# Optimization experiments

Measured on AMD Instinct MI355X. Metric: run time of the kernel, lower is better.

## Reference

```python
import jax, jax.numpy as jnp
import numpy as np

SEQ, BATCH, HIDDEN, VOCAB = 2048, 2, 4096, 32000

def setup_inputs() -> dict:
    key = jax.random.key(0)
    k1, k2, k3 = jax.random.split(key, 3)
    hidden_states = jax.random.normal(k1, (SEQ, BATCH, HIDDEN), dtype=jnp.float32)
    weight = jax.random.normal(k2, (VOCAB, HIDDEN), dtype=jnp.float32) * (HIDDEN ** -0.5)
    labels = jax.random.randint(k3, (BATCH, SEQ), 0, VOCAB, dtype=jnp.int64)
    return {"hidden_states": hidden_states, "weight": weight, "labels": labels}

def reference(hidden_states, weight, labels):
    # LM head: [s,b,h] @ [v,h]^T -> [s,b,v]
    logits = jnp.einsum('sbh,vh->sbv', hidden_states, weight)
    labels_sb = labels.T  # [b,s] -> [s,b] to match logits layout
    # per-token cross entropy (vocab-parallel CE with world_size=1)
    logp = jax.nn.log_softmax(logits, axis=-1)
    nll = -jnp.take_along_axis(logp, labels_sb[..., None], axis=-1)[..., 0]  # [s,b]
    return nll.T  # [b,s], matching final loss.transpose(0,1)
```

## Files before the change

kernel.cpp:

```cpp
#include <hip/hip_runtime.h>
#include <hip/hip_bf16.h>
#include <stdint.h>

#define SEQ 2048
#define HID 4096
#define VOCAB 32000
#define MTOK 4096
#define NCHUNK 500

typedef __attribute__((ext_vector_type(8))) short short8v;
typedef __attribute__((ext_vector_type(4))) float float4v;

__device__ __forceinline__ short f2bf(float x) {
    unsigned u = __float_as_uint(x);
    u += 0x7fff + ((u >> 16) & 1);
    return (short)(u >> 16);
}

__global__ __launch_bounds__(256) void cvt_f32_bf16(const float* __restrict__ in,
                                                    short* __restrict__ out, int n8) {
    int stride = gridDim.x * 256;
    for (int i = blockIdx.x * 256 + threadIdx.x; i < n8; i += stride) {
        float4 a = *(const float4*)(in + (size_t)i * 8);
        float4 b = *(const float4*)(in + (size_t)i * 8 + 4);
        short8v v = { f2bf(a.x), f2bf(a.y), f2bf(a.z), f2bf(a.w),
                      f2bf(b.x), f2bf(b.y), f2bf(b.z), f2bf(b.w) };
        *(short8v*)(out + (size_t)i * 8) = v;
    }
}

__global__ __launch_bounds__(256) void gemm_ce_bf(
    const short* __restrict__ A, const short* __restrict__ B,
    const int* __restrict__ labels, float2* __restrict__ partials,
    float* __restrict__ labelv)
{
    const int bid = blockIdx.x;
    const int mb = bid & 31;
    const int nb = bid >> 5;
    const int tid = threadIdx.x;
    const int lane = tid & 63;
    const int wid = tid >> 6;
    const int wm = wid >> 1, wn = wid & 1;
    const int l15 = lane & 15;
    const int l4  = lane >> 4;

    __shared__ short As[128 * 64];
    __shared__ short Bs[128 * 64];

    float4v acc[4][4];
    #pragma unroll
    for (int i = 0; i < 4; i++)
        #pragma unroll
        for (int j = 0; j < 4; j++) acc[i][j] = (float4v){0.f, 0.f, 0.f, 0.f};

    const int srow = tid >> 3;
    const int scol = ((tid & 7) ^ (srow & 7)) * 8;
    const short* aptr = A + (size_t)(mb * 128 + srow) * HID + scol;
    const short* bptr = B + (size_t)(nb * 128 + srow) * HID + scol;

    for (int k0 = 0; k0 < HID; k0 += 64) {
        __syncthreads();
        #pragma unroll
        for (int r = 0; r < 4; r++) {
            __builtin_amdgcn_global_load_lds(
                (const __attribute__((address_space(1))) unsigned int*)(aptr + (size_t)r * 32 * HID + k0),
                (__attribute__((address_space(3))) unsigned int*)(As + ((r * 256 + wid * 64) * 8)),
                16, 0, 0);
            __builtin_amdgcn_global_load_lds(
                (const __attribute__((address_space(1))) unsigned int*)(bptr + (size_t)r * 32 * HID + k0),
                (__attribute__((address_space(3))) unsigned int*)(Bs + ((r * 256 + wid * 64) * 8)),
                16, 0, 0);
        }
        __syncthreads();
        #pragma unroll
        for (int kk = 0; kk < 64; kk += 32) {
            const int cA = (((kk >> 3) + l4) ^ (l15 & 7)) * 8;
            short8v a[4], b[4];
            #pragma unroll
            for (int i = 0; i < 4; i++)
                a[i] = *(const short8v*)&As[(wm * 64 + i * 16 + l15) * 64 + cA];
            #pragma unroll
            for (int i = 0; i < 4; i++)
                b[i] = *(const short8v*)&Bs[(wn * 64 + i * 16 + l15) * 64 + cA];
            #pragma unroll
            for (int i = 0; i < 4; i++)
                #pragma unroll
                for (int j = 0; j < 4; j++)
                    acc[i][j] = __builtin_amdgcn_mfma_f32_16x16x32_bf16(
                        a[i], b[j], acc[i][j], 0, 0, 0);
        }
    }

    #pragma unroll
    for (int mi = 0; mi < 4; mi++) {
        #pragma unroll
        for (int j = 0; j < 4; j++) {
            int token = mb * 128 + wm * 64 + mi * 16 + l4 * 4 + j;
            float v0 = acc[mi][0][j], v1 = acc[mi][1][j];
            float v2 = acc[mi][2][j], v3 = acc[mi][3][j];
            float mx = fmaxf(fmaxf(v0, v1), fmaxf(v2, v3));
            #pragma unroll
            for (int d = 1; d < 16; d <<= 1) mx = fmaxf(mx, __shfl_xor(mx, d));
            float sum = expf(v0 - mx) + expf(v1 - mx) + expf(v2 - mx) + expf(v3 - mx);
            #pragma unroll
            for (int d = 1; d < 16; d <<= 1) sum += __shfl_xor(sum, d);
            int chunk = nb * 2 + wn;
            if (l15 == 0)
                partials[(size_t)token * NCHUNK + chunk] = make_float2(mx, sum);
            int lab = labels[(token & 1) * SEQ + (token >> 1)];
            int cbase = nb * 128 + wn * 64 + l15;
            #pragma unroll
            for (int ni = 0; ni < 4; ni++)
                if (cbase + ni * 16 == lab)
                    labelv[token] = (ni == 0 ? v0 : ni == 1 ? v1 : ni == 2 ? v2 : v3);
        }
    }
}

__global__ __launch_bounds__(256) void gemm_ce_phase1(
    const float* __restrict__ hid, const float* __restrict__ w,
    const int* __restrict__ labels, float2* __restrict__ partials,
    float* __restrict__ labelv)
{
    const int bid = blockIdx.x;
    const int mb = bid & 31;
    const int nb = bid >> 5;
    const int tid = threadIdx.x;
    const int lane = tid & 63;
    const int wid = tid >> 6;
    const int wm = wid >> 1, wn = wid & 1;
    const int l15 = lane & 15;
    const int l4  = lane >> 4;

    __shared__ short As[128][72];
    __shared__ short Bs[128][72];

    float4v acc[4][4];
    #pragma unroll
    for (int i = 0; i < 4; i++)
        #pragma unroll
        for (int j = 0; j < 4; j++) acc[i][j] = (float4v){0.f, 0.f, 0.f, 0.f};

    const int srow = tid >> 3;
    const int scol = (tid & 7) * 8;
    const float* aptr = hid + (size_t)(mb * 128 + srow) * HID + scol;
    const float* bptr = w   + (size_t)(nb * 128 + srow) * HID + scol;

    for (int k0 = 0; k0 < HID; k0 += 64) {
        __syncthreads();
        #pragma unroll
        for (int r = 0; r < 4; r++) {
            const float* ap = aptr + (size_t)r * 32 * HID + k0;
            const float* bp = bptr + (size_t)r * 32 * HID + k0;
            float4 a0 = *(const float4*)ap;
            float4 a1 = *(const float4*)(ap + 4);
            float4 b0 = *(const float4*)bp;
            float4 b1 = *(const float4*)(bp + 4);
            short8v av = { f2bf(a0.x), f2bf(a0.y), f2bf(a0.z), f2bf(a0.w),
                           f2bf(a1.x), f2bf(a1.y), f2bf(a1.z), f2bf(a1.w) };
            short8v bv = { f2bf(b0.x), f2bf(b0.y), f2bf(b0.z), f2bf(b0.w),
                           f2bf(b1.x), f2bf(b1.y), f2bf(b1.z), f2bf(b1.w) };
            *(short8v*)&As[srow + r * 32][scol] = av;
            *(short8v*)&Bs[srow + r * 32][scol] = bv;
        }
        __syncthreads();
        const int kb = l4 * 8;
        #pragma unroll
        for (int kk = 0; kk < 64; kk += 32) {
            short8v a[4], b[4];
            #pragma unroll
            for (int i = 0; i < 4; i++)
                a[i] = *(const short8v*)&As[wm * 64 + i * 16 + l15][kk + kb];
            #pragma unroll
            for (int i = 0; i < 4; i++)
                b[i] = *(const short8v*)&Bs[wn * 64 + i * 16 + l15][kk + kb];
            #pragma unroll
            for (int i = 0; i < 4; i++)
                #pragma unroll
                for (int j = 0; j < 4; j++)
                    acc[i][j] = __builtin_amdgcn_mfma_f32_16x16x32_bf16(
                        a[i], b[j], acc[i][j], 0, 0, 0);
        }
    }

    #pragma unroll
    for (int mi = 0; mi < 4; mi++) {
        #pragma unroll
        for (int j = 0; j < 4; j++) {
            int token = mb * 128 + wm * 64 + mi * 16 + l4 * 4 + j;
            float v0 = acc[mi][0][j], v1 = acc[mi][1][j];
            float v2 = acc[mi][2][j], v3 = acc[mi][3][j];
            float mx = fmaxf(fmaxf(v0, v1), fmaxf(v2, v3));
            #pragma unroll
            for (int d = 1; d < 16; d <<= 1) mx = fmaxf(mx, __shfl_xor(mx, d));
            float sum = expf(v0 - mx) + expf(v1 - mx) + expf(v2 - mx) + expf(v3 - mx);
            #pragma unroll
            for (int d = 1; d < 16; d <<= 1) sum += __shfl_xor(sum, d);
            int chunk = nb * 2 + wn;
            if (l15 == 0)
                partials[(size_t)token * NCHUNK + chunk] = make_float2(mx, sum);
            int lab = labels[(token & 1) * SEQ + (token >> 1)];
            int cbase = nb * 128 + wn * 64 + l15;
            #pragma unroll
            for (int ni = 0; ni < 4; ni++)
                if (cbase + ni * 16 == lab)
                    labelv[token] = (ni == 0 ? v0 : ni == 1 ? v1 : ni == 2 ? v2 : v3);
        }
    }
}

__global__ __launch_bounds__(256) void ce_phase2(
    const float2* __restrict__ partials, const float* __restrict__ labelv,
    float* __restrict__ out)
{
    int token = blockIdx.x * 4 + (threadIdx.x >> 6);
    int lane = threadIdx.x & 63;
    float m = -INFINITY, s = 0.f;
    for (int i = lane; i < NCHUNK; i += 64) {
        float2 p = partials[(size_t)token * NCHUNK + i];
        float nm = fmaxf(m, p.x);
        s = s * expf(m - nm) + p.y * expf(p.x - nm);
        m = nm;
    }
    #pragma unroll
    for (int d = 1; d < 64; d <<= 1) {
        float om = __shfl_xor(m, d);
        float os = __shfl_xor(s, d);
        float nm = fmaxf(m, om);
        s = s * expf(m - nm) + os * expf(om - nm);
        m = nm;
    }
    if (lane == 0) {
        float nll = m + logf(s) - labelv[token];
        out[(token & 1) * SEQ + (token >> 1)] = nll;
    }
}

extern "C" void kernel_launch(void* const* d_in, const int* in_sizes, int n_in,
                              void* d_out, int out_size, void* d_ws, size_t ws_size,
                              hipStream_t stream) {
    const float* hid = (const float*)d_in[0];
    const float* w   = (const float*)d_in[1];
    const int* labels = (const int*)d_in[2];
    float* out = (float*)d_out;

    const size_t WBF  = (size_t)VOCAB * HID * sizeof(short);
    const size_t HBF  = (size_t)MTOK * HID * sizeof(short);
    const size_t PART = (size_t)MTOK * NCHUNK * sizeof(float2);
    const size_t LABV = (size_t)MTOK * sizeof(float);

    if (ws_size >= WBF + HBF + PART + LABV) {
        short* wbf = (short*)d_ws;
        short* hbf = (short*)((char*)d_ws + WBF);
        float2* partials = (float2*)((char*)d_ws + WBF + HBF);
        float* labelv = (float*)((char*)d_ws + WBF + HBF + PART);
        cvt_f32_bf16<<<dim3(2048), dim3(256), 0, stream>>>(w, wbf, VOCAB * HID / 8);
        cvt_f32_bf16<<<dim3(2048), dim3(256), 0, stream>>>(hid, hbf, MTOK * HID / 8);
        gemm_ce_bf<<<dim3(32 * 250), dim3(256), 0, stream>>>(hbf, wbf, labels, partials, labelv);
        ce_phase2<<<dim3(MTOK / 4), dim3(256), 0, stream>>>(partials, labelv, out);
    } else {
        float2* partials = (float2*)d_ws;
        float* labelv = (float*)((char*)d_ws + PART);
        gemm_ce_phase1<<<dim3(32 * 250), dim3(256), 0, stream>>>(hid, w, labels, partials, labelv);
        ce_phase2<<<dim3(MTOK / 4), dim3(256), 0, stream>>>(partials, labelv, out);
    }
}
```

Measured before the change: 1.611 ms.

## Double-buffer LDS tiles with async prefetch, swizzle block order, raise MFMA priority

Adds a two-stage LDS ping-pong so the next K tile's global_load_lds is issued before computing the current one. Partial vmcnt waits let that load overlap the MFMA work. Block IDs are remapped so consecutive blocks land on different XCDs and neighbouring blocks share weight tiles, aiming for better L2 reuse. s_setprio is raised around the MFMA burst. The cost is doubled LDS use (64KB), which may reduce occupancy, and a hand-tuned waitcnt count that must match the number of issued loads.

Result: slower. 1.706 ms (+5.9%).

```diff
diff --git a/kernel.cpp b/kernel.cpp
--- a/kernel.cpp
+++ b/kernel.cpp
@@ -34,7 +34,7 @@
     const int* __restrict__ labels, float2* __restrict__ partials,
     float* __restrict__ labelv)
 {
-    const int bid = blockIdx.x;
+    const int bid = (blockIdx.x & 7) * 1000 + (blockIdx.x >> 3);
     const int mb = bid & 31;
     const int nb = bid >> 5;
     const int tid = threadIdx.x;
@@ -44,8 +44,8 @@
     const int l15 = lane & 15;
     const int l4  = lane >> 4;
 
-    __shared__ short As[128 * 64];
-    __shared__ short Bs[128 * 64];
+    __shared__ short As[2][128 * 64];
+    __shared__ short Bs[2][128 * 64];
 
     float4v acc[4][4];
     #pragma unroll
@@ -58,36 +58,52 @@
     const short* aptr = A + (size_t)(mb * 128 + srow) * HID + scol;
     const short* bptr = B + (size_t)(nb * 128 + srow) * HID + scol;
 
-    for (int k0 = 0; k0 < HID; k0 += 64) {
-        __syncthreads();
-        #pragma unroll
-        for (int r = 0; r < 4; r++) {
-            __builtin_amdgcn_global_load_lds(
-                (const __attribute__((address_space(1))) unsigned int*)(aptr + (size_t)r * 32 * HID + k0),
-                (__attribute__((address_space(3))) unsigned int*)(As + ((r * 256 + wid * 64) * 8)),
-                16, 0, 0);
-            __builtin_amdgcn_global_load_lds(
-                (const __attribute__((address_space(1))) unsigned int*)(bptr + (size_t)r * 32 * HID + k0),
-                (__attribute__((address_space(3))) unsigned int*)(Bs + ((r * 256 + wid * 64) * 8)),
-                16, 0, 0);
-        }
-        __syncthreads();
+    #define STAGE(T, BUF)                                                              \
+        _Pragma("unroll")                                                              \
+        for (int r = 0; r < 4; r++) {                                                  \
+            __builtin_amdgcn_global_load_lds(                                          \
+                (const __attribute__((address_space(1))) unsigned int*)(aptr + (size_t)r * 32 * HID + (T) * 64), \
+                (__attribute__((address_space(3))) unsigned int*)(&As[BUF][0] + ((r * 256 + wid * 64) * 8)),     \
+                16, 0, 0);                                                             \
+            __builtin_amdgcn_global_load_lds(                                          \
+                (const __attribute__((address_space(1))) unsigned int*)(bptr + (size_t)r * 32 * HID + (T) * 64), \
+                (__attribute__((address_space(3))) unsigned int*)(&Bs[BUF][0] + ((r * 256 + wid * 64) * 8)),     \
+                16, 0, 0);                                                             \
+        }
+
+    STAGE(0, 0);
+
+    for (int t = 0; t < 64; ++t) {
+        __builtin_amdgcn_s_barrier();
+        if (t < 63) {
+            STAGE(t + 1, (t + 1) & 1);
+            asm volatile("s_waitcnt vmcnt(8)" ::: "memory");
+        } else {
+            asm volatile("s_waitcnt vmcnt(0)" ::: "memory");
+        }
+        __builtin_amdgcn_s_barrier();
+        __builtin_amdgcn_sched_barrier(0);
+
+        const short* as = &As[t & 1][0];
+        const short* bs = &Bs[t & 1][0];
         #pragma unroll
         for (int kk = 0; kk < 64; kk += 32) {
             const int cA = (((kk >> 3) + l4) ^ (l15 & 7)) * 8;
             short8v a[4], b[4];
             #pragma unroll
             for (int i = 0; i < 4; i++)
-                a[i] = *(const short8v*)&As[(wm * 64 + i * 16 + l15) * 64 + cA];
-            #pragma unroll
-            for (int i = 0; i < 4; i++)
-                b[i] = *(const short8v*)&Bs[(wn * 64 + i * 16 + l15) * 64 + cA];
+                a[i] = *(const short8v*)&as[(wm * 64 + i * 16 + l15) * 64 + cA];
+            #pragma unroll
+            for (int i = 0; i < 4; i++)
+                b[i] = *(const short8v*)&bs[(wn * 64 + i * 16 + l15) * 64 + cA];
+            __builtin_amdgcn_s_setprio(1);
             #pragma unroll
             for (int i = 0; i < 4; i++)
                 #pragma unroll
                 for (int j = 0; j < 4; j++)
                     acc[i][j] = __builtin_amdgcn_mfma_f32_16x16x32_bf16(
                         a[i], b[j], acc[i][j], 0, 0, 0);
+            __builtin_amdgcn_s_setprio(0);
         }
     }
 
```
